# Kernel tuning notes

Measured on AMD Instinct MI355X. Metric: run time of the kernel, lower is better.

## Reference

```python
import jax, jax.numpy as jnp
import numpy as np

B, N, C, L = 32, 1024, 1024, 16  # batch, pixels (HW), channels, visual tokens


def setup_inputs() -> dict:
    key = jax.random.key(0)
    ks = jax.random.split(key, 18)
    s = lambda fan_in: 1.0 / np.sqrt(fan_in)
    def lin(kw, kb, fin, fout):
        W = jax.random.uniform(kw, (fin, fout), jnp.float32, -s(fin), s(fin))
        b = jax.random.uniform(kb, (fout,), jnp.float32, -s(fin), s(fin))
        return W, b
    tok_W, tok_b = lin(ks[0], ks[1], C, L)          # tokenizer pointwise conv
    key_W, key_b = lin(ks[2], ks[3], C, C // 2)     # transformer key proj
    query_W, query_b = lin(ks[4], ks[5], C, C // 2) # transformer query proj
    f1_W, f1_b = lin(ks[6], ks[7], C, C)            # FFN 1
    f2_W, f2_b = lin(ks[8], ks[9], C, C)            # FFN 2
    q_W, q_b = lin(ks[10], ks[11], C, C)            # projector W_q
    k_W, k_b = lin(ks[12], ks[13], C, C)            # projector W_k
    feature_map = jax.random.normal(ks[14], (B, N, C), jnp.float32)
    T_in = jnp.zeros((B, L, C), jnp.float32)  # unused by FilterBasedTokenizer
    return dict(feature_map=feature_map, T_in=T_in,
                tok_W=tok_W, tok_b=tok_b, key_W=key_W, key_b=key_b,
                query_W=query_W, query_b=query_b, f1_W=f1_W, f1_b=f1_b,
                f2_W=f2_W, f2_b=f2_b, q_W=q_W, q_b=q_b, k_W=k_W, k_b=k_b)


def reference(feature_map, T_in, tok_W, tok_b, key_W, key_b, query_W, query_b,
              f1_W, f1_b, f2_W, f2_b, q_W, q_b, k_W, k_b):
    X = feature_map  # [B, N, C]
    # --- FilterBasedTokenizer: softmax over pixel dim, aggregate pixels -> tokens
    proj = X @ tok_W + tok_b                         # [B, N, L]
    attn = jax.nn.softmax(proj, axis=1)              # softmax over N (dim=1)
    T = jnp.einsum('bnl,bnc->blc', attn, X)          # [B, L, C]
    # --- Transformer block on visual tokens
    k = T @ key_W + key_b                            # [B, L, C/2]
    q = T @ query_W + query_b                        # [B, L, C/2]
    scores = jnp.einsum('bld,bmd->blm', k, q)        # [B, L, L]
    T_dash = T + jax.nn.softmax(scores, axis=2) @ T  # self-attn residual
    T_out = T_dash + (jax.nn.relu(T_dash @ f1_W + f1_b) @ f2_W + f2_b)
    # --- Projector: pixels attend to tokens
    sim = jnp.einsum('bnc,blc->bnl', X @ q_W + q_b, T_out @ k_W + k_b)  # [B, N, L]
    X_out = X + jax.nn.softmax(sim, axis=2) @ T_out  # [B, N, C]
    return (X_out, T_out)
```

## Files before the change

### kernel.cpp

```cpp
#include <hip/hip_runtime.h>
#include <hip/hip_bf16.h>
#include <stdint.h>

#define BB 32
#define NN 1024
#define CC 1024
#define LL 16

typedef __attribute__((ext_vector_type(4))) float f32x4;
typedef __attribute__((ext_vector_type(8))) short short8;
typedef __attribute__((ext_vector_type(4))) unsigned short ushort4v;

__device__ __forceinline__ unsigned short f2bf(float f) {
  union { float f; unsigned u; } v; v.f = f;
  unsigned r = v.u + 0x7FFF + ((v.u >> 16) & 1);
  return (unsigned short)(r >> 16);
}
__device__ __forceinline__ float bf2f(unsigned short h) {
  union { unsigned u; float f; } v; v.u = ((unsigned)h) << 16; return v.f;
}

__global__ __launch_bounds__(256) void wprep(
    const float* __restrict__ keyW, const float* __restrict__ queryW,
    const float* __restrict__ f1W, const float* __restrict__ f2W,
    const float* __restrict__ kW, const float* __restrict__ qW,
    unsigned short* __restrict__ WkqT, unsigned short* __restrict__ f1WT,
    unsigned short* __restrict__ f2WT, unsigned short* __restrict__ kWT,
    unsigned short* __restrict__ qWbf)
{
  int z = blockIdx.z;
  int tx = threadIdx.x, ty = threadIdx.y;
  if (z == 4) {
#pragma unroll
    for (int i = 0; i < 4; ++i) {
      int row = blockIdx.y * 32 + ty + 8 * i;
      int col = blockIdx.x * 32 + tx;
      qWbf[row * 1024 + col] = f2bf(qW[row * 1024 + col]);
    }
    return;
  }
  __shared__ float tile[32][33];
  int j0 = blockIdx.x * 32, k0 = blockIdx.y * 32;
  const float* src = (z == 1) ? f1W : (z == 2) ? f2W : kW;
#pragma unroll
  for (int i = 0; i < 4; ++i) {
    int k = k0 + ty + 8 * i;
    int j = j0 + tx;
    float v;
    if (z == 0) v = (j < 512) ? keyW[k * 512 + j] : queryW[k * 512 + (j - 512)];
    else        v = src[k * 1024 + j];
    tile[ty + 8 * i][tx] = v;
  }
  __syncthreads();
  unsigned short* dst = (z == 0) ? WkqT : (z == 1) ? f1WT : (z == 2) ? f2WT : kWT;
#pragma unroll
  for (int i = 0; i < 4; ++i) {
    int j = j0 + ty + 8 * i;
    dst[j * 1024 + k0 + tx] = f2bf(tile[tx][ty + 8 * i]);
  }
}

__global__ void tokprep(const float* __restrict__ tokW, unsigned short* __restrict__ tokWT) {
  int i = blockIdx.x * 256 + threadIdx.x;
  int l = i >> 10, c = i & 1023;
  tokWT[i] = f2bf(tokW[c * 16 + l]);
}

__global__ void bias_pack(const float* __restrict__ keyb,
                          const float* __restrict__ queryb,
                          float* __restrict__ biaskq) {
  int i = blockIdx.x * 256 + threadIdx.x;
  biaskq[i] = (i < 512) ? keyb[i] : queryb[i - 512];
}

template<int IS_SIM>
__global__ __launch_bounds__(256) void pix_mfma(
    const float* __restrict__ X, const unsigned short* __restrict__ Wt,
    const float* __restrict__ bias, float* __restrict__ out)
{
  __shared__ __align__(16) char sp[16384];
  int tid = threadIdx.x, wid = tid >> 6, lane = tid & 63;
  int lr = lane & 15, hi = lane >> 4;
  int pix0 = blockIdx.x * 64 + blockIdx.y * 1024;
  int b = pix0 >> 10;
  int row = tid >> 2, seg = tid & 3;
  const float* xr = X + (size_t)(pix0 + row) * 1024 + seg * 32;
  const unsigned short* Wb = Wt + (IS_SIM ? ((size_t)b * 16 * 1024) : (size_t)0)
                             + (size_t)lr * 1024 + hi * 8;
  int wbyte[4];
#pragma unroll
  for (int u = 0; u < 4; ++u)
    wbyte[u] = row * 256 + (((seg * 64 + u * 16) ^ ((row & 7) << 4)));
  int arow = wid * 16 + lr;
  int rbyte = arow * 256;
  int rx = (arow & 7) << 4;
  f32x4 acc = (f32x4)0.f;
  for (int k0 = 0; k0 < 1024; k0 += 128) {
    f32x4 v[8];
#pragma unroll
    for (int i = 0; i < 8; ++i) v[i] = *(const f32x4*)(xr + k0 + i * 4);
    __syncthreads();
#pragma unroll
    for (int u = 0; u < 4; ++u) {
      short8 pk;
      pk[0] = (short)f2bf(v[2*u][0]);   pk[1] = (short)f2bf(v[2*u][1]);
      pk[2] = (short)f2bf(v[2*u][2]);   pk[3] = (short)f2bf(v[2*u][3]);
      pk[4] = (short)f2bf(v[2*u+1][0]); pk[5] = (short)f2bf(v[2*u+1][1]);
      pk[6] = (short)f2bf(v[2*u+1][2]); pk[7] = (short)f2bf(v[2*u+1][3]);
      *(short8*)(sp + wbyte[u]) = pk;
    }
    __syncthreads();
#pragma unroll
    for (int kk = 0; kk < 4; ++kk) {
      short8 af = *(const short8*)(sp + rbyte + (((kk * 64 + hi * 16) ^ rx)));
      short8 bf = *(const short8*)(Wb + k0 + kk * 32);
      acc = __builtin_amdgcn_mfma_f32_16x16x32_bf16(af, bf, acc, 0, 0, 0);
    }
  }
  int pixb = pix0 + wid * 16 + hi * 4;
  if (!IS_SIM) {
    float bv = bias[lr];
#pragma unroll
    for (int rr = 0; rr < 4; ++rr) {
      int pix = pixb + rr;
      out[((size_t)b * 16 + lr) * 1024 + (pix & 1023)] = acc[rr] + bv;
    }
  } else {
    float bv = bias[b * 16 + lr];
#pragma unroll
    for (int rr = 0; rr < 4; ++rr) {
      float vv = acc[rr] + bv;
      float mx = vv;
      mx = fmaxf(mx, __shfl_xor(mx, 1)); mx = fmaxf(mx, __shfl_xor(mx, 2));
      mx = fmaxf(mx, __shfl_xor(mx, 4)); mx = fmaxf(mx, __shfl_xor(mx, 8));
      float e = __expf(vv - mx);
      float ss = e;
      ss += __shfl_xor(ss, 1); ss += __shfl_xor(ss, 2);
      ss += __shfl_xor(ss, 4); ss += __shfl_xor(ss, 8);
      out[(size_t)(pixb + rr) * 16 + lr] = e / ss;
    }
  }
}

__global__ __launch_bounds__(256) void softmax_n(float* __restrict__ projT) {
  float* row = projT + (size_t)blockIdx.x * NN;
  int t = threadIdx.x;
  f32x4 v = ((f32x4*)row)[t];
  float m = fmaxf(fmaxf(v[0], v[1]), fmaxf(v[2], v[3]));
#pragma unroll
  for (int msk = 32; msk >= 1; msk >>= 1) m = fmaxf(m, __shfl_xor(m, msk));
  __shared__ float redm[4], reds[4];
  if ((t & 63) == 0) redm[t >> 6] = m;
  __syncthreads();
  m = fmaxf(fmaxf(redm[0], redm[1]), fmaxf(redm[2], redm[3]));
  f32x4 e;
  e[0] = __expf(v[0] - m); e[1] = __expf(v[1] - m);
  e[2] = __expf(v[2] - m); e[3] = __expf(v[3] - m);
  float s = e[0] + e[1] + e[2] + e[3];
#pragma unroll
  for (int msk = 32; msk >= 1; msk >>= 1) s += __shfl_xor(s, msk);
  if ((t & 63) == 0) reds[t >> 6] = s;
  __syncthreads();
  s = reds[0] + reds[1] + reds[2] + reds[3];
  float inv = 1.f / s;
  e[0] *= inv; e[1] *= inv; e[2] *= inv; e[3] *= inv;
  ((f32x4*)row)[t] = e;
}

__global__ __launch_bounds__(256) void tpart_kernel(
    const float* __restrict__ X, const float* __restrict__ attnT,
    unsigned short* __restrict__ TpartBf)
{
  int b = blockIdx.y, ch = blockIdx.x;
  int n0 = ch * 64;
  __shared__ float att[64][16];
  int tid = threadIdx.x;
  {
    int l = tid >> 4, n4 = (tid & 15) * 4;
    f32x4 a = *(const f32x4*)&attnT[((size_t)b * 16 + l) * 1024 + n0 + n4];
    att[n4 + 0][l] = a[0]; att[n4 + 1][l] = a[1];
    att[n4 + 2][l] = a[2]; att[n4 + 3][l] = a[3];
  }
  __syncthreads();
  f32x4 acc[16];
#pragma unroll
  for (int l = 0; l < 16; ++l) acc[l] = (f32x4)0.f;
  const float* xp = X + ((size_t)b * 1024 + n0) * 1024 + tid * 4;
#pragma unroll 4
  for (int n = 0; n < 64; ++n) {
    f32x4 xv = *(const f32x4*)(xp + (size_t)n * 1024);
    const f32x4* ar = (const f32x4*)&att[n][0];
    f32x4 a0 = ar[0], a1 = ar[1], a2 = ar[2], a3 = ar[3];
    acc[0]  += a0[0]*xv; acc[1]  += a0[1]*xv; acc[2]  += a0[2]*xv; acc[3]  += a0[3]*xv;
    acc[4]  += a1[0]*xv; acc[5]  += a1[1]*xv; acc[6]  += a1[2]*xv; acc[7]  += a1[3]*xv;
    acc[8]  += a2[0]*xv; acc[9]  += a2[1]*xv; acc[10] += a2[2]*xv; acc[11] += a2[3]*xv;
    acc[12] += a3[0]*xv; acc[13] += a3[1]*xv; acc[14] += a3[2]*xv; acc[15] += a3[3]*xv;
  }
  unsigned short* op = TpartBf + (size_t)(b * 16 + ch) * 16 * 1024 + tid * 4;
#pragma unroll
  for (int l = 0; l < 16; ++l) {
    f32x4 s = acc[l];
    ushort4v h; h[0]=f2bf(s[0]); h[1]=f2bf(s[1]); h[2]=f2bf(s[2]); h[3]=f2bf(s[3]);
    *(ushort4v*)(op + (size_t)l * 1024) = h;
  }
}

__global__ void treduce(const unsigned short* __restrict__ TpartBf,
                        float* __restrict__ T, unsigned short* __restrict__ Tbf) {
  int f = blockIdx.x * 256 + threadIdx.x;
  int b = f >> 12, w = f & 4095;
  f32x4 s = (f32x4)0.f;
#pragma unroll
  for (int ch = 0; ch < 16; ++ch) {
    ushort4v h = ((const ushort4v*)TpartBf)[(size_t)(b * 16 + ch) * 4096 + w];
    s[0] += bf2f(h[0]); s[1] += bf2f(h[1]); s[2] += bf2f(h[2]); s[3] += bf2f(h[3]);
  }
  ((f32x4*)T)[f] = s;
  ushort4v h; h[0]=f2bf(s[0]); h[1]=f2bf(s[1]); h[2]=f2bf(s[2]); h[3]=f2bf(s[3]);
  ((ushort4v*)Tbf)[f] = h;
}

template<int RELU, int HAS_BIAS, int HAS_RES, int STORE_F32, int STORE_BF16>
__global__ __launch_bounds__(256) void gemm32x64(
    const unsigned short* __restrict__ A, const unsigned short* __restrict__ Bm,
    const float* __restrict__ bias, const float* __restrict__ res,
    float* __restrict__ outF, unsigned short* __restrict__ outB)
{
  const int K = 1024;
  __shared__ __align__(16) char sh[12288];
  char* Asp = sh;
  char* Bsp = sh + 4096;
  int tid = threadIdx.x, wid = tid >> 6, lane = tid & 63;
  int lr = lane & 15, hi = lane >> 4;
  int m0 = blockIdx.x * 32, n0 = blockIdx.y * 64;
  int arow = tid >> 3, acol = (tid & 7) * 8;
  int brow = tid >> 2, bcol = (tid & 3) * 16;
  const unsigned short* Ap = A + (size_t)(m0 + arow) * K + acol;
  const unsigned short* Bp = Bm + (size_t)(n0 + brow) * K + bcol;
  int aw  = arow * 128 + (((acol * 2) ^ ((arow & 7) << 4)));
  int bw0 = brow * 128 + (((bcol * 2) ^ ((brow & 7) << 4)));
  int bw1 = brow * 128 + ((((bcol * 2) + 16) ^ ((brow & 7) << 4)));
  short8 aR[2]; short8 bR[2][2];
  aR[0]    = *(const short8*)(Ap);
  bR[0][0] = *(const short8*)(Bp);
  bR[0][1] = *(const short8*)(Bp + 8);
  aR[1]    = *(const short8*)(Ap + 64);
  bR[1][0] = *(const short8*)(Bp + 64);
  bR[1][1] = *(const short8*)(Bp + 72);
  f32x4 acc[2];
  acc[0] = (f32x4)0.f; acc[1] = (f32x4)0.f;
  int wm = (wid >> 1) * 16, wn = (wid & 1) * 32;
  int arb = (wm + lr) * 128, arx = ((wm + lr) & 7) << 4;
  for (int s = 0; s < 16; ++s) {
    __syncthreads();
    *(short8*)(Asp + aw)  = aR[s & 1];
    *(short8*)(Bsp + bw0) = bR[s & 1][0];
    *(short8*)(Bsp + bw1) = bR[s & 1][1];
    __syncthreads();
    if (s + 2 < 16) {
      int k0 = (s + 2) * 64;
      aR[s & 1]    = *(const short8*)(Ap + k0);
      bR[s & 1][0] = *(const short8*)(Bp + k0);
      bR[s & 1][1] = *(const short8*)(Bp + k0 + 8);
    }
#pragma unroll
    for (int kk = 0; kk < 2; ++kk) {
      short8 af = *(const short8*)(Asp + arb + (((kk * 64 + hi * 16) ^ arx)));
#pragma unroll
      for (int sn = 0; sn < 2; ++sn) {
        int br = wn + sn * 16 + lr;
        short8 bf = *(const short8*)(Bsp + br * 128 + (((kk * 64 + hi * 16) ^ ((br & 7) << 4))));
        acc[sn] = __builtin_amdgcn_mfma_f32_16x16x32_bf16(af, bf, acc[sn], 0, 0, 0);
      }
    }
  }
  int row0 = m0 + wm + hi * 4;
#pragma unroll
  for (int sn = 0; sn < 2; ++sn) {
    int col = n0 + wn + sn * 16 + lr;
    float bv_ = HAS_BIAS ? bias[col] : 0.f;
#pragma unroll
    for (int rr = 0; rr < 4; ++rr) {
      float x = acc[sn][rr] + bv_;
      if (RELU) x = fmaxf(x, 0.f);
      size_t idx = (size_t)(row0 + rr) * 1024 + col;
      if (HAS_RES) x += res[idx];
      if (STORE_F32) outF[idx] = x;
      if (STORE_BF16) outB[idx] = f2bf(x);
    }
  }
}

__global__ __launch_bounds__(256) void scores_tdash(
    const float* __restrict__ kq, const float* __restrict__ T,
    float* __restrict__ Tdash, unsigned short* __restrict__ Tdbf)
{
  int cs = blockIdx.x, b = blockIdx.y;
  int c0 = cs * 128;
  __shared__ float Ts[16][128];
  int tid = threadIdx.x, lane = tid & 63;
#pragma unroll
  for (int i = 0; i < 2; ++i) {
    int fi = tid + 256 * i;
    int rrow = fi >> 5, c4 = (fi & 31) * 4;
    *(f32x4*)&Ts[rrow][c4] = *(const f32x4*)&T[((size_t)b * 16 + rrow) * 1024 + c0 + c4];
  }
  __syncthreads();
  int l = tid >> 4, m = tid & 15;
  const float* krow = kq + ((size_t)b * 16 + l) * 1024;
  const float* qrow = kq + ((size_t)b * 16 + m) * 1024 + 512;
  float s = 0.f;
#pragma unroll 8
  for (int d = 0; d < 512; d += 4) {
    f32x4 kv = *(const f32x4*)(krow + d);
    f32x4 qv = *(const f32x4*)(qrow + d);
    s += kv[0]*qv[0] + kv[1]*qv[1] + kv[2]*qv[2] + kv[3]*qv[3];
  }
  float mx = s;
  mx = fmaxf(mx, __shfl_xor(mx, 1)); mx = fmaxf(mx, __shfl_xor(mx, 2));
  mx = fmaxf(mx, __shfl_xor(mx, 4)); mx = fmaxf(mx, __shfl_xor(mx, 8));
  float e = __expf(s - mx);
  float sum = e;
  sum += __shfl_xor(sum, 1); sum += __shfl_xor(sum, 2);
  sum += __shfl_xor(sum, 4); sum += __shfl_xor(sum, 8);
  float pv = e / sum;
  float pl[16];
#pragma unroll
  for (int i = 0; i < 16; ++i) pl[i] = __shfl(pv, (lane & 48) + i);
  float* od = Tdash + ((size_t)b * 16 + l) * 1024 + c0;
  unsigned short* ob = Tdbf + ((size_t)b * 16 + l) * 1024 + c0;
#pragma unroll
  for (int h = 0; h < 2; ++h) {
    int c = m * 8 + h * 4;
    f32x4 o = *(const f32x4*)&Ts[l][c];
#pragma unroll
    for (int mm = 0; mm < 16; ++mm) {
      f32x4 tv = *(const f32x4*)&Ts[mm][c];
      o += pl[mm] * tv;
    }
    *(f32x4*)(od + c) = o;
    ushort4v hh; hh[0]=f2bf(o[0]); hh[1]=f2bf(o[1]); hh[2]=f2bf(o[2]); hh[3]=f2bf(o[3]);
    *(ushort4v*)(ob + c) = hh;
  }
}

__global__ __launch_bounds__(256) void r_kernel(
    const unsigned short* __restrict__ Tkbf, const float* __restrict__ qb,
    float* __restrict__ r)
{
  int row = blockIdx.x * 4 + (threadIdx.x >> 6);
  int lane = threadIdx.x & 63;
  const unsigned short* p = Tkbf + (size_t)row * CC;
  float s = 0.f;
#pragma unroll
  for (int h = 0; h < 2; ++h) {
    int d0 = lane * 8 + h * 512;
    short8 v = *(const short8*)&p[d0];
#pragma unroll
    for (int jj = 0; jj < 8; ++jj)
      s += bf2f((unsigned short)v[jj]) * qb[d0 + jj];
  }
#pragma unroll
  for (int msk = 32; msk >= 1; msk >>= 1) s += __shfl_xor(s, msk);
  if (lane == 0) r[row] = s;
}

__global__ __launch_bounds__(256) void out_kernel(
    const float* __restrict__ X, const float* __restrict__ P,
    const float* __restrict__ Tout, float* __restrict__ Xout)
{
  int b = blockIdx.y, ch = blockIdx.x;
  int tid = threadIdx.x;
  int c4 = tid * 4;
  f32x4 tsr[16];
#pragma unroll
  for (int l = 0; l < 16; ++l)
    tsr[l] = *(const f32x4*)&Tout[((size_t)b * 16 + l) * 1024 + c4];
  __shared__ float Ps[64][16];
  {
    int px = tid >> 2, q = (tid & 3) * 4;
    *(f32x4*)&Ps[px][q] = *(const f32x4*)&P[(size_t)(b * 1024 + ch * 64 + px) * 16 + q];
  }
  __syncthreads();
  const float* xp = X + ((size_t)b * 1024 + ch * 64) * 1024 + c4;
  float* op = Xout + ((size_t)b * 1024 + ch * 64) * 1024 + c4;
#pragma unroll 2
  for (int n = 0; n < 64; ++n) {
    f32x4 xv = *(const f32x4*)(xp + (size_t)n * 1024);
    const f32x4* pr = (const f32x4*)&Ps[n][0];
    f32x4 p0 = pr[0], p1 = pr[1], p2 = pr[2], p3 = pr[3];
    f32x4 o = xv;
    o += p0[0]*tsr[0];  o += p0[1]*tsr[1];  o += p0[2]*tsr[2];  o += p0[3]*tsr[3];
    o += p1[0]*tsr[4];  o += p1[1]*tsr[5];  o += p1[2]*tsr[6];  o += p1[3]*tsr[7];
    o += p2[0]*tsr[8];  o += p2[1]*tsr[9];  o += p2[2]*tsr[10]; o += p2[3]*tsr[11];
    o += p3[0]*tsr[12]; o += p3[1]*tsr[13]; o += p3[2]*tsr[14]; o += p3[3]*tsr[15];
    *(f32x4*)(op + (size_t)n * 1024) = o;
  }
}

extern "C" void kernel_launch(void* const* d_in, const int* in_sizes, int n_in,
                              void* d_out, int out_size, void* d_ws, size_t ws_size,
                              hipStream_t stream)
{
  const float* X      = (const float*)d_in[0];
  const float* tokW   = (const float*)d_in[2];
  const float* tokB   = (const float*)d_in[3];
  const float* keyW   = (const float*)d_in[4];
  const float* keyB   = (const float*)d_in[5];
  const float* queryW = (const float*)d_in[6];
  const float* queryB = (const float*)d_in[7];
  const float* f1W    = (const float*)d_in[8];
  const float* f1B    = (const float*)d_in[9];
  const float* f2W    = (const float*)d_in[10];
  const float* f2B    = (const float*)d_in[11];
  const float* qW     = (const float*)d_in[12];
  const float* qB     = (const float*)d_in[13];
  const float* kW     = (const float*)d_in[14];
  const float* kB     = (const float*)d_in[15];

  float* Xout = (float*)d_out;
  float* Tout = (float*)d_out + (size_t)BB * NN * CC;

  char* ws = (char*)d_ws;
  size_t off = 0;
  auto alloc_f = [&](size_t n) { float* pp = (float*)(ws + off); off += n * 4; return pp; };
  float* attn   = alloc_f(524288);
  float* Tbuf   = alloc_f(524288);
  float* kqbuf  = alloc_f(524288);
  float* Tdash  = alloc_f(524288);
  float* Pbuf   = alloc_f(524288);
  float* rbuf   = alloc_f(1024);
  float* biaskq = alloc_f(1024);
  auto alloc_h = [&](size_t n) { unsigned short* pp = (unsigned short*)(ws + off); off += n * 2; return pp; };
  unsigned short* TpartBf = alloc_h(8388608);
  unsigned short* Tbf    = alloc_h(524288);
  unsigned short* Tdbf   = alloc_h(524288);
  unsigned short* Hbf    = alloc_h(524288);
  unsigned short* Toutbf = alloc_h(524288);
  unsigned short* Tkbf   = alloc_h(524288);
  unsigned short* Gtbf   = alloc_h(524288);
  unsigned short* WkqT   = alloc_h(1048576);
  unsigned short* f1WT   = alloc_h(1048576);
  unsigned short* f2WT   = alloc_h(1048576);
  unsigned short* kWT    = alloc_h(1048576);
  unsigned short* qWbf   = alloc_h(1048576);
  unsigned short* tokWT  = alloc_h(16384);
  (void)ws_size; (void)in_sizes; (void)n_in; (void)out_size;

  wprep<<<dim3(32, 32, 5), dim3(32, 8), 0, stream>>>(keyW, queryW, f1W, f2W, kW, qW,
                                                     WkqT, f1WT, f2WT, kWT, qWbf);
  tokprep<<<64, 256, 0, stream>>>(tokW, tokWT);
  bias_pack<<<4, 256, 0, stream>>>(keyB, queryB, biaskq);
  pix_mfma<0><<<dim3(512, 1), 256, 0, stream>>>(X, tokWT, tokB, attn);
  softmax_n<<<512, 256, 0, stream>>>(attn);
  tpart_kernel<<<dim3(16, 32), 256, 0, stream>>>(X, attn, TpartBf);
  treduce<<<512, 256, 0, stream>>>(TpartBf, Tbuf, Tbf);
  gemm32x64<0,1,0,1,0><<<dim3(16, 16), 256, 0, stream>>>(Tbf, WkqT, biaskq, nullptr, kqbuf, nullptr);
  scores_tdash<<<dim3(8, 32), 256, 0, stream>>>(kqbuf, Tbuf, Tdash, Tdbf);
  gemm32x64<1,1,0,0,1><<<dim3(16, 16), 256, 0, stream>>>(Tdbf, f1WT, f1B, nullptr, nullptr, Hbf);
  gemm32x64<0,1,1,1,1><<<dim3(16, 16), 256, 0, stream>>>(Hbf, f2WT, f2B, Tdash, Tout, Toutbf);
  gemm32x64<0,1,0,0,1><<<dim3(16, 16), 256, 0, stream>>>(Toutbf, kWT, kB, nullptr, nullptr, Tkbf);
  r_kernel<<<128, 256, 0, stream>>>(Tkbf, qB, rbuf);
  gemm32x64<0,0,0,0,1><<<dim3(16, 16), 256, 0, stream>>>(Tkbf, qWbf, nullptr, nullptr, nullptr, Gtbf);
  pix_mfma<1><<<dim3(16, 32), 256, 0, stream>>>(X, Gtbf, rbuf, Pbuf);
  out_kernel<<<dim3(16, 32), 256, 0, stream>>>(X, Pbuf, Tout, Xout);
}
```

Measured before the change: 211.9 us.

## Fuse projector sim-softmax into output kernel, merge prep kernels, halve T partials

Merges the sim MFMA/softmax kernel with the output kernel, so each block computes its 64 pixels' token probabilities into shared memory and then writes X_out directly. This removes the P buffer round-trip and one launch. The tokenizer-weight and bias packing are folded into the weight-prep launch as an extra z slice. The T partial kernel now covers 128 pixels per block, which halves the partial buffer and the reduce work but gives fewer blocks (256) for parallelism. The fused kernel re-reads X rows that its MFMA stage just streamed, so cache reuse may help, while longer blocks may reduce overlap.

```diff
diff --git a/kernel.cpp b/kernel.cpp
--- a/kernel.cpp
+++ b/kernel.cpp
@@ -24,12 +24,26 @@
     const float* __restrict__ keyW, const float* __restrict__ queryW,
     const float* __restrict__ f1W, const float* __restrict__ f2W,
     const float* __restrict__ kW, const float* __restrict__ qW,
+    const float* __restrict__ tokW, const float* __restrict__ keyb,
+    const float* __restrict__ queryb,
     unsigned short* __restrict__ WkqT, unsigned short* __restrict__ f1WT,
     unsigned short* __restrict__ f2WT, unsigned short* __restrict__ kWT,
-    unsigned short* __restrict__ qWbf)
+    unsigned short* __restrict__ qWbf, unsigned short* __restrict__ tokWT,
+    float* __restrict__ biaskq)
 {
   int z = blockIdx.z;
   int tx = threadIdx.x, ty = threadIdx.y;
+  if (z == 5) {
+    int gid = (blockIdx.y * 32 + blockIdx.x) * 256 + ty * 32 + tx;
+    if (gid < 16384) {
+      int l = gid >> 10, c = gid & 1023;
+      tokWT[gid] = f2bf(tokW[c * 16 + l]);
+    } else if (gid < 17408) {
+      int i = gid - 16384;
+      biaskq[i] = (i < 512) ? keyb[i] : queryb[i - 512];
+    }
+    return;
+  }
   if (z == 4) {
 #pragma unroll
     for (int i = 0; i < 4; ++i) {
@@ -60,33 +74,18 @@
   }
 }
 
-__global__ void tokprep(const float* __restrict__ tokW, unsigned short* __restrict__ tokWT) {
-  int i = blockIdx.x * 256 + threadIdx.x;
-  int l = i >> 10, c = i & 1023;
-  tokWT[i] = f2bf(tokW[c * 16 + l]);
-}
-
-__global__ void bias_pack(const float* __restrict__ keyb,
-                          const float* __restrict__ queryb,
-                          float* __restrict__ biaskq) {
-  int i = blockIdx.x * 256 + threadIdx.x;
-  biaskq[i] = (i < 512) ? keyb[i] : queryb[i - 512];
-}
-
-template<int IS_SIM>
-__global__ __launch_bounds__(256) void pix_mfma(
+__global__ __launch_bounds__(256) void proj_mfma(
     const float* __restrict__ X, const unsigned short* __restrict__ Wt,
     const float* __restrict__ bias, float* __restrict__ out)
 {
   __shared__ __align__(16) char sp[16384];
   int tid = threadIdx.x, wid = tid >> 6, lane = tid & 63;
   int lr = lane & 15, hi = lane >> 4;
-  int pix0 = blockIdx.x * 64 + blockIdx.y * 1024;
+  int pix0 = blockIdx.x * 64;
   int b = pix0 >> 10;
   int row = tid >> 2, seg = tid & 3;
   const float* xr = X + (size_t)(pix0 + row) * 1024 + seg * 32;
-  const unsigned short* Wb = Wt + (IS_SIM ? ((size_t)b * 16 * 1024) : (size_t)0)
-                             + (size_t)lr * 1024 + hi * 8;
+  const unsigned short* Wb = Wt + (size_t)lr * 1024 + hi * 8;
   int wbyte[4];
 #pragma unroll
   for (int u = 0; u < 4; ++u)
@@ -118,27 +117,11 @@
     }
   }
   int pixb = pix0 + wid * 16 + hi * 4;
-  if (!IS_SIM) {
-    float bv = bias[lr];
-#pragma unroll
-    for (int rr = 0; rr < 4; ++rr) {
-      int pix = pixb + rr;
-      out[((size_t)b * 16 + lr) * 1024 + (pix & 1023)] = acc[rr] + bv;
-    }
-  } else {
-    float bv = bias[b * 16 + lr];
-#pragma unroll
-    for (int rr = 0; rr < 4; ++rr) {
-      float vv = acc[rr] + bv;
-      float mx = vv;
-      mx = fmaxf(mx, __shfl_xor(mx, 1)); mx = fmaxf(mx, __shfl_xor(mx, 2));
-      mx = fmaxf(mx, __shfl_xor(mx, 4)); mx = fmaxf(mx, __shfl_xor(mx, 8));
-      float e = __expf(vv - mx);
-      float ss = e;
-      ss += __shfl_xor(ss, 1); ss += __shfl_xor(ss, 2);
-      ss += __shfl_xor(ss, 4); ss += __shfl_xor(ss, 8);
-      out[(size_t)(pixb + rr) * 16 + lr] = e / ss;
-    }
+  float bv = bias[lr];
+#pragma unroll
+  for (int rr = 0; rr < 4; ++rr) {
+    int pix = pixb + rr;
+    out[((size_t)b * 16 + lr) * 1024 + (pix & 1023)] = acc[rr] + bv;
   }
 }
 
@@ -172,11 +155,13 @@
     unsigned short* __restrict__ TpartBf)
 {
   int b = blockIdx.y, ch = blockIdx.x;
-  int n0 = ch * 64;
-  __shared__ float att[64][16];
+  int n0 = ch * 128;
+  __shared__ float att[128][16];
   int tid = threadIdx.x;
-  {
-    int l = tid >> 4, n4 = (tid & 15) * 4;
+#pragma unroll
+  for (int i = 0; i < 2; ++i) {
+    int fi = tid + 256 * i;
+    int l = fi >> 5, n4 = (fi & 31) << 2;
     f32x4 a = *(const f32x4*)&attnT[((size_t)b * 16 + l) * 1024 + n0 + n4];
     att[n4 + 0][l] = a[0]; att[n4 + 1][l] = a[1];
     att[n4 + 2][l] = a[2]; att[n4 + 3][l] = a[3];
@@ -187,7 +172,7 @@
   for (int l = 0; l < 16; ++l) acc[l] = (f32x4)0.f;
   const float* xp = X + ((size_t)b * 1024 + n0) * 1024 + tid * 4;
 #pragma unroll 4
-  for (int n = 0; n < 64; ++n) {
+  for (int n = 0; n < 128; ++n) {
     f32x4 xv = *(const f32x4*)(xp + (size_t)n * 1024);
     const f32x4* ar = (const f32x4*)&att[n][0];
     f32x4 a0 = ar[0], a1 = ar[1], a2 = ar[2], a3 = ar[3];
@@ -196,7 +181,7 @@
     acc[8]  += a2[0]*xv; acc[9]  += a2[1]*xv; acc[10] += a2[2]*xv; acc[11] += a2[3]*xv;
     acc[12] += a3[0]*xv; acc[13] += a3[1]*xv; acc[14] += a3[2]*xv; acc[15] += a3[3]*xv;
   }
-  unsigned short* op = TpartBf + (size_t)(b * 16 + ch) * 16 * 1024 + tid * 4;
+  unsigned short* op = TpartBf + (size_t)(b * 8 + ch) * 16 * 1024 + tid * 4;
 #pragma unroll
   for (int l = 0; l < 16; ++l) {
     f32x4 s = acc[l];
@@ -211,8 +196,8 @@
   int b = f >> 12, w = f & 4095;
   f32x4 s = (f32x4)0.f;
 #pragma unroll
-  for (int ch = 0; ch < 16; ++ch) {
-    ushort4v h = ((const ushort4v*)TpartBf)[(size_t)(b * 16 + ch) * 4096 + w];
+  for (int ch = 0; ch < 8; ++ch) {
+    ushort4v h = ((const ushort4v*)TpartBf)[(size_t)(b * 8 + ch) * 4096 + w];
     s[0] += bf2f(h[0]); s[1] += bf2f(h[1]); s[2] += bf2f(h[2]); s[3] += bf2f(h[3]);
   }
   ((f32x4*)T)[f] = s;
@@ -365,25 +350,72 @@
   if (lane == 0) r[row] = s;
 }
 
-__global__ __launch_bounds__(256) void out_kernel(
-    const float* __restrict__ X, const float* __restrict__ P,
-    const float* __restrict__ Tout, float* __restrict__ Xout)
-{
-  int b = blockIdx.y, ch = blockIdx.x;
-  int tid = threadIdx.x;
+__global__ __launch_bounds__(256) void sim_out_kernel(
+    const float* __restrict__ X, const unsigned short* __restrict__ Gt,
+    const float* __restrict__ rbias, const float* __restrict__ Tout,
+    float* __restrict__ Xout)
+{
+  __shared__ __align__(16) char sp[16384];
+  __shared__ float Ps[64][16];
+  int tid = threadIdx.x, wid = tid >> 6, lane = tid & 63;
+  int lr = lane & 15, hi = lane >> 4;
+  int pix0 = blockIdx.x * 64 + blockIdx.y * 1024;
+  int b = blockIdx.y;
+  int row = tid >> 2, seg = tid & 3;
+  const float* xr = X + (size_t)(pix0 + row) * 1024 + seg * 32;
+  const unsigned short* Wb = Gt + (size_t)b * 16 * 1024 + (size_t)lr * 1024 + hi * 8;
+  int wbyte[4];
+#pragma unroll
+  for (int u = 0; u < 4; ++u)
+    wbyte[u] = row * 256 + (((seg * 64 + u * 16) ^ ((row & 7) << 4)));
+  int arow = wid * 16 + lr;
+  int rbyte = arow * 256;
+  int rx = (arow & 7) << 4;
+  f32x4 acc = (f32x4)0.f;
+  for (int k0 = 0; k0 < 1024; k0 += 128) {
+    f32x4 v[8];
+#pragma unroll
+    for (int i = 0; i < 8; ++i) v[i] = *(const f32x4*)(xr + k0 + i * 4);
+    __syncthreads();
+#pragma unroll
+    for (int u = 0; u < 4; ++u) {
+      short8 pk;
+      pk[0] = (short)f2bf(v[2*u][0]);   pk[1] = (short)f2bf(v[2*u][1]);
+      pk[2] = (short)f2bf(v[2*u][2]);   pk[3] = (short)f2bf(v[2*u][3]);
+      pk[4] = (short)f2bf(v[2*u+1][0]); pk[5] = (short)f2bf(v[2*u+1][1]);
+      pk[6] = (short)f2bf(v[2*u+1][2]); pk[7] = (short)f2bf(v[2*u+1][3]);
+      *(short8*)(sp + wbyte[u]) = pk;
+    }
+    __syncthreads();
+#pragma unroll
+    for (int kk = 0; kk < 4; ++kk) {
+      short8 af = *(const short8*)(sp + rbyte + (((kk * 64 + hi * 16) ^ rx)));
+      short8 bf = *(const short8*)(Wb + k0 + kk * 32);
+      acc = __builtin_amdgcn_mfma_f32_16x16x32_bf16(af, bf, acc, 0, 0, 0);
+    }
+  }
+  float bv = rbias[b * 16 + lr];
+  int prow = wid * 16 + hi * 4;
+#pragma unroll
+  for (int rr = 0; rr < 4; ++rr) {
+    float vv = acc[rr] + bv;
+    float mx = vv;
+    mx = fmaxf(mx, __shfl_xor(mx, 1)); mx = fmaxf(mx, __shfl_xor(mx, 2));
+    mx = fmaxf(mx, __shfl_xor(mx, 4)); mx = fmaxf(mx, __shfl_xor(mx, 8));
+    float e = __expf(vv - mx);
+    float ss = e;
+    ss += __shfl_xor(ss, 1); ss += __shfl_xor(ss, 2);
+    ss += __shfl_xor(ss, 4); ss += __shfl_xor(ss, 8);
+    Ps[prow + rr][lr] = e / ss;
+  }
+  __syncthreads();
   int c4 = tid * 4;
   f32x4 tsr[16];
 #pragma unroll
   for (int l = 0; l < 16; ++l)
     tsr[l] = *(const f32x4*)&Tout[((size_t)b * 16 + l) * 1024 + c4];
-  __shared__ float Ps[64][16];
-  {
-    int px = tid >> 2, q = (tid & 3) * 4;
-    *(f32x4*)&Ps[px][q] = *(const f32x4*)&P[(size_t)(b * 1024 + ch * 64 + px) * 16 + q];
-  }
-  __syncthreads();
-  const float* xp = X + ((size_t)b * 1024 + ch * 64) * 1024 + c4;
-  float* op = Xout + ((size_t)b * 1024 + ch * 64) * 1024 + c4;
+  const float* xp = X + (size_t)pix0 * 1024 + c4;
+  float* op = Xout + (size_t)pix0 * 1024 + c4;
 #pragma unroll 2
   for (int n = 0; n < 64; ++n) {
     f32x4 xv = *(const f32x4*)(xp + (size_t)n * 1024);
@@ -428,11 +460,10 @@
   float* Tbuf   = alloc_f(524288);
   float* kqbuf  = alloc_f(524288);
   float* Tdash  = alloc_f(524288);
-  float* Pbuf   = alloc_f(524288);
   float* rbuf   = alloc_f(1024);
   float* biaskq = alloc_f(1024);
   auto alloc_h = [&](size_t n) { unsigned short* pp = (unsigned short*)(ws + off); off += n * 2; return pp; };
-  unsigned short* TpartBf = alloc_h(8388608);
+  unsigned short* TpartBf = alloc_h(4194304);
   unsigned short* Tbf    = alloc_h(524288);
   unsigned short* Tdbf   = alloc_h(524288);
   unsigned short* Hbf    = alloc_h(524288);
@@ -447,13 +478,12 @@
   unsigned short* tokWT  = alloc_h(16384);
   (void)ws_size; (void)in_sizes; (void)n_in; (void)out_size;
 
-  wprep<<<dim3(32, 32, 5), dim3(32, 8), 0, stream>>>(keyW, queryW, f1W, f2W, kW, qW,
-                                                     WkqT, f1WT, f2WT, kWT, qWbf);
-  tokprep<<<64, 256, 0, stream>>>(tokW, tokWT);
-  bias_pack<<<4, 256, 0, stream>>>(keyB, queryB, biaskq);
-  pix_mfma<0><<<dim3(512, 1), 256, 0, stream>>>(X, tokWT, tokB, attn);
+  wprep<<<dim3(32, 32, 6), dim3(32, 8), 0, stream>>>(keyW, queryW, f1W, f2W, kW, qW,
+                                                     tokW, keyB, queryB,
+                                                     WkqT, f1WT, f2WT, kWT, qWbf, tokWT, biaskq);
+  proj_mfma<<<dim3(512), 256, 0, stream>>>(X, tokWT, tokB, attn);
   softmax_n<<<512, 256, 0, stream>>>(attn);
-  tpart_kernel<<<dim3(16, 32), 256, 0, stream>>>(X, attn, TpartBf);
+  tpart_kernel<<<dim3(8, 32), 256, 0, stream>>>(X, attn, TpartBf);
   treduce<<<512, 256, 0, stream>>>(TpartBf, Tbuf, Tbf);
   gemm32x64<0,1,0,1,0><<<dim3(16, 16), 256, 0, stream>>>(Tbf, WkqT, biaskq, nullptr, kqbuf, nullptr);
   scores_tdash<<<dim3(8, 32), 256, 0, stream>>>(kqbuf, Tbuf, Tdash, Tdbf);
@@ -462,6 +492,5 @@
   gemm32x64<0,1,0,0,1><<<dim3(16, 16), 256, 0, stream>>>(Toutbf, kWT, kB, nullptr, nullptr, Tkbf);
   r_kernel<<<128, 256, 0, stream>>>(Tkbf, qB, rbuf);
   gemm32x64<0,0,0,0,1><<<dim3(16, 16), 256, 0, stream>>>(Tkbf, qWbf, nullptr, nullptr, nullptr, Gtbf);
-  pix_mfma<1><<<dim3(16, 32), 256, 0, stream>>>(X, Gtbf, rbuf, Pbuf);
-  out_kernel<<<dim3(16, 32), 256, 0, stream>>>(X, Pbuf, Tout, Xout);
-}
+  sim_out_kernel<<<dim3(16, 32), 256, 0, stream>>>(X, Gtbf, rbuf, Tout, Xout);
+}
```

After: 210.6 us. About the same (-0.6%).
